# Performance work log

Measured on AMD Instinct MI355X. Metric: run time of the kernel, lower is better.

The kernel has to match this reference:

```python
import jax, jax.numpy as jnp
import numpy as np

B, T, C, H, W = 16, 128, 32, 16, 16
NUM_FEAT = 16
D = C * H * W            # conv1d in-channels (kernel size 1 => linear)
G = NUM_FEAT * H * W     # G3 out-channels


def setup_inputs() -> dict:
    key = jax.random.key(0)
    ks = jax.random.split(key, 8)
    s1 = 1.0 / np.sqrt(D)
    return {
        "input1": jax.random.normal(ks[0], (B, T, C, H, W), jnp.float32),
        "input2": jax.random.normal(ks[1], (B, T, C, H, W), jnp.float32),
        "w1": jax.random.uniform(ks[2], (NUM_FEAT, D), jnp.float32, -s1, s1),
        "b1": jax.random.uniform(ks[3], (NUM_FEAT,), jnp.float32, -s1, s1),
        "w2": jax.random.uniform(ks[4], (NUM_FEAT, D), jnp.float32, -s1, s1),
        "b2": jax.random.uniform(ks[5], (NUM_FEAT,), jnp.float32, -s1, s1),
        "w3": jax.random.uniform(ks[6], (G, D), jnp.float32, -s1, s1),
        "b3": jax.random.uniform(ks[7], (G,), jnp.float32, -s1, s1),
    }


def reference(input1, input2, w1, b1, w2, b2, w3, b3):
    b, t = input1.shape[:2]
    x1 = input1.reshape(b, t, D)  # [B,T,D]
    x2 = input2.reshape(b, t, D)
    # Conv1d(kernel=1) projections (channels-first conv == per-frame linear)
    q = jnp.einsum('btd,fd->btf', x1, w1) + b1          # [B,T,F]
    k = jnp.einsum('bsd,fd->bsf', x2, w2) + b2          # [B,S,F]
    scores = jnp.einsum('btf,bsf->bts', q, k)            # [B,T,T]
    attn = jax.nn.softmax(scores, axis=1)                # softmax over dim=1 (rows)
    v = jnp.einsum('bsd,gd->bsg', x1, w3) + b3           # [B,T,G]
    out = jnp.einsum('bts,bsg->btg', attn, v)            # [B,T,G]
    return out.reshape(b, t, NUM_FEAT, H, W)
```

## Files before the change

kernel.cpp:

```cpp
#include <hip/hip_runtime.h>
#include <cstdint>
#include <cstddef>

#define Bn 16
#define Tn 128
#define Dn 8192
#define Fn 16
#define Gn 4096
#define MT (Bn*Tn)

#define QKP 4

typedef __attribute__((ext_vector_type(8))) short short8;
typedef __attribute__((ext_vector_type(4))) float f32x4;

__device__ inline short f2bf(float f) {
    union { float f; uint32_t u; } c; c.f = f;
    uint32_t u = c.u;
    uint32_t r = (u + 0x7FFFu + ((u >> 16) & 1u)) >> 16;
    return (short)(r & 0xFFFFu);
}

__device__ inline short8 cvt8(float4 a, float4 b) {
    short8 v;
    v[0] = f2bf(a.x); v[1] = f2bf(a.y); v[2] = f2bf(a.z); v[3] = f2bf(a.w);
    v[4] = f2bf(b.x); v[5] = f2bf(b.y); v[6] = f2bf(b.z); v[7] = f2bf(b.w);
    return v;
}

#define N8_X1 (MT * Dn / 8)
#define N8_W3 ((size_t)Gn * Dn / 8)

__global__ __launch_bounds__(256) void cvt2_kernel(
    const float* __restrict__ x1, const float* __restrict__ w3,
    short* __restrict__ x1b, short* __restrict__ w3b)
{
    const size_t total = N8_X1 + N8_W3;
    size_t i = (size_t)blockIdx.x * 256 + threadIdx.x;
    const size_t stride = (size_t)gridDim.x * 256;
    for (; i < total; i += stride) {
        if (i < N8_X1) {
            const float4* s = ((const float4*)x1) + i * 2;
            ((short8*)x1b)[i] = cvt8(s[0], s[1]);
        } else {
            const size_t j = i - N8_X1;
            const float4* s = ((const float4*)w3) + j * 2;
            ((short8*)w3b)[j] = cvt8(s[0], s[1]);
        }
    }
}

__global__ __launch_bounds__(256) void qk_gemm_kernel(
    const short* __restrict__ x1b, const float* __restrict__ x2,
    const float* __restrict__ w1, const float* __restrict__ w2,
    float* __restrict__ qp, float* __restrict__ kp)
{
    __shared__ float red[4][16][16];
    const int tid = threadIdx.x;
    const int tile = blockIdx.x >> 1;
    const int isK  = blockIdx.x & 1;
    const int kq   = blockIdx.y;
    const int m0 = tile * 16;
    const int wave = tid >> 6, lane = tid & 63;
    const int quad = lane >> 4, r = lane & 15;
    const int kbase = kq * (Dn / QKP) + wave * (Dn / QKP / 4);

    f32x4 acc = {};

    if (!isK) {
        const short* ap = x1b + (size_t)(m0 + r) * Dn + kbase + quad * 8;
        const float* bp = w1 + (size_t)r * Dn + kbase + quad * 8;
        #pragma unroll 4
        for (int it = 0; it < 16; ++it) {
            short8 af = *(const short8*)(ap + it * 32);
            const float4* b4 = (const float4*)(bp + it * 32);
            short8 bf = cvt8(b4[0], b4[1]);
            acc = __builtin_amdgcn_mfma_f32_16x16x32_bf16(af, bf, acc, 0, 0, 0);
        }
    } else {
        const float* apf = x2 + (size_t)(m0 + r) * Dn + kbase + quad * 8;
        const float* bp  = w2 + (size_t)r * Dn + kbase + quad * 8;
        #pragma unroll 4
        for (int it = 0; it < 16; ++it) {
            const float4* a4 = (const float4*)(apf + it * 32);
            short8 af = cvt8(a4[0], a4[1]);
            const float4* b4 = (const float4*)(bp + it * 32);
            short8 bf = cvt8(b4[0], b4[1]);
            acc = __builtin_amdgcn_mfma_f32_16x16x32_bf16(af, bf, acc, 0, 0, 0);
        }
    }

    #pragma unroll
    for (int reg = 0; reg < 4; ++reg)
        red[wave][quad * 4 + reg][r] = acc[reg];
    __syncthreads();

    const int m = tid >> 4, f = tid & 15;
    float s = red[0][m][f] + red[1][m][f] + red[2][m][f] + red[3][m][f];
    float* dst = isK ? kp : qp;
    dst[((size_t)kq * MT + m0 + m) * Fn + f] = s;
}

__global__ __launch_bounds__(256) void attn_kernel(
    const float* __restrict__ qp, const float* __restrict__ kp,
    const float* __restrict__ b1, const float* __restrict__ b2,
    short* __restrict__ attn16)
{
    __shared__ float qs[Tn * 17];
    const int b = blockIdx.x;
    const int tid = threadIdx.x;
    const int wave = tid >> 6, lane = tid & 63;
    const int s = blockIdx.y * 4 + wave;

    for (int i = tid; i < Tn * Fn; i += 256) {
        float v = b1[i & 15];
        #pragma unroll
        for (int p = 0; p < QKP; ++p)
            v += qp[(size_t)p * MT * Fn + b * Tn * Fn + i];
        qs[(i >> 4) * 17 + (i & 15)] = v;
    }
    __syncthreads();

    float kr[16];
    #pragma unroll
    for (int f = 0; f < 16; ++f) {
        float v = b2[f];
        #pragma unroll
        for (int p = 0; p < QKP; ++p)
            v += kp[((size_t)p * MT + b * Tn + s) * Fn + f];
        kr[f] = v;
    }

    const int t0 = lane, t1 = lane + 64;
    float sc0 = 0.f, sc1 = 0.f;
    #pragma unroll
    for (int f = 0; f < 16; ++f) {
        sc0 += qs[t0 * 17 + f] * kr[f];
        sc1 += qs[t1 * 17 + f] * kr[f];
    }
    float m = fmaxf(sc0, sc1);
    #pragma unroll
    for (int off = 32; off > 0; off >>= 1)
        m = fmaxf(m, __shfl_xor(m, off, 64));
    const float e0 = __expf(sc0 - m), e1 = __expf(sc1 - m);
    float ssum = e0 + e1;
    #pragma unroll
    for (int off = 32; off > 0; off >>= 1)
        ssum += __shfl_xor(ssum, off, 64);
    const float inv = 1.f / ssum;

    short* ap = attn16 + (size_t)b * Tn * Tn;
    ap[t0 * Tn + s] = f2bf(e0 * inv);
    ap[t1 * Tn + s] = f2bf(e1 * inv);
}

#define BK 32

__global__ __launch_bounds__(256) void gemm_v_split_kernel(
    const short* __restrict__ A, const short* __restrict__ Bw,
    float* __restrict__ vTf, const int kspan)
{
    __shared__ __attribute__((aligned(16))) short As[128 * BK];
    __shared__ __attribute__((aligned(16))) short Bs[128 * BK];

    const int tid = threadIdx.x;
    const int m0 = blockIdx.y * 128;
    const int n0 = blockIdx.x * 128;
    const int z  = blockIdx.z;
    const int kbase = z * kspan;
    float* outp = vTf + (size_t)z * Gn * MT;
    const int wave = tid >> 6, lane = tid & 63;
    const int wm = (wave >> 1) * 64, wn = (wave & 1) * 64;
    const int quad = lane >> 4, r = lane & 15;

    const int srow = wave * 32 + (lane >> 2);
    const int scol = (lane & 3) * 8;
    const short* gA = A  + (size_t)(m0 + srow) * Dn + kbase + scol;
    const short* gB = Bw + (size_t)(n0 + srow) * Dn + kbase + scol;
    short* lA = &As[srow * BK + scol];
    short* lB = &Bs[srow * BK + scol];

    f32x4 acc[4][4] = {};

    #pragma unroll 1
    for (int k0 = 0; k0 < kspan; k0 += BK) {
        __syncthreads();
        __builtin_amdgcn_global_load_lds(
            (const __attribute__((address_space(1))) void*)(gA + k0),
            (__attribute__((address_space(3))) void*)lA, 16, 0, 0);
        __builtin_amdgcn_global_load_lds(
            (const __attribute__((address_space(1))) void*)(gA + k0 + (size_t)16 * Dn),
            (__attribute__((address_space(3))) void*)(lA + 16 * BK), 16, 0, 0);
        __builtin_amdgcn_global_load_lds(
            (const __attribute__((address_space(1))) void*)(gB + k0),
            (__attribute__((address_space(3))) void*)lB, 16, 0, 0);
        __builtin_amdgcn_global_load_lds(
            (const __attribute__((address_space(1))) void*)(gB + k0 + (size_t)16 * Dn),
            (__attribute__((address_space(3))) void*)(lB + 16 * BK), 16, 0, 0);
        __syncthreads();

        short8 af[4], bf[4];
        #pragma unroll
        for (int i = 0; i < 4; ++i)
            af[i] = *(const short8*)&As[(wm + i * 16 + r) * BK + quad * 8];
        #pragma unroll
        for (int j = 0; j < 4; ++j)
            bf[j] = *(const short8*)&Bs[(wn + j * 16 + r) * BK + quad * 8];

        #pragma unroll
        for (int i = 0; i < 4; ++i)
            #pragma unroll
            for (int j = 0; j < 4; ++j)
                acc[i][j] = __builtin_amdgcn_mfma_f32_16x16x32_bf16(
                    af[i], bf[j], acc[i][j], 0, 0, 0);
    }

    #pragma unroll
    for (int i = 0; i < 4; ++i) {
        #pragma unroll
        for (int reg = 0; reg < 4; ++reg) {
            const int rowg = m0 + wm + i * 16 + quad * 4 + reg;
            #pragma unroll
            for (int j = 0; j < 4; ++j) {
                const int col = n0 + wn + j * 16 + r;
                outp[(size_t)rowg * MT + col] = acc[i][j][reg];
            }
        }
    }
}

__global__ __launch_bounds__(256) void vt_cvt_kernel(
    const float* __restrict__ vTf, const float* __restrict__ bias,
    short* __restrict__ vT, const int nparts)
{
    const size_t N8 = (size_t)Gn * MT / 8;
    size_t i = (size_t)blockIdx.x * 256 + threadIdx.x;
    const size_t stride = (size_t)gridDim.x * 256;
    for (; i < N8; i += stride) {
        const float bv = bias[i >> 8];
        float4 a = {bv, bv, bv, bv}, b = {bv, bv, bv, bv};
        for (int p = 0; p < nparts; ++p) {
            const float4* pp = (const float4*)(vTf + (size_t)p * Gn * MT);
            float4 a1 = pp[i * 2], b1 = pp[i * 2 + 1];
            a.x += a1.x; a.y += a1.y; a.z += a1.z; a.w += a1.w;
            b.x += b1.x; b.y += b1.y; b.z += b1.z; b.w += b1.w;
        }
        ((short8*)vT)[i] = cvt8(a, b);
    }
}

__global__ __launch_bounds__(256) void gemm_v_kernel(
    const short* __restrict__ A, const short* __restrict__ Bw,
    const float* __restrict__ bias, short* __restrict__ vT)
{
    __shared__ __attribute__((aligned(16))) short As[128 * BK];
    __shared__ __attribute__((aligned(16))) short Bs[128 * BK];

    const int tid = threadIdx.x;
    const int m0 = blockIdx.y * 128;
    const int n0 = blockIdx.x * 128;
    const int wave = tid >> 6, lane = tid & 63;
    const int wm = (wave >> 1) * 64, wn = (wave & 1) * 64;
    const int quad = lane >> 4, r = lane & 15;

    const int srow = wave * 32 + (lane >> 2);
    const int scol = (lane & 3) * 8;
    const short* gA = A  + (size_t)(m0 + srow) * Dn + scol;
    const short* gB = Bw + (size_t)(n0 + srow) * Dn + scol;
    short* lA = &As[srow * BK + scol];
    short* lB = &Bs[srow * BK + scol];

    f32x4 acc[4][4] = {};

    #pragma unroll 1
    for (int k0 = 0; k0 < Dn; k0 += BK) {
        __syncthreads();
        __builtin_amdgcn_global_load_lds(
            (const __attribute__((address_space(1))) void*)(gA + k0),
            (__attribute__((address_space(3))) void*)lA, 16, 0, 0);
        __builtin_amdgcn_global_load_lds(
            (const __attribute__((address_space(1))) void*)(gA + k0 + (size_t)16 * Dn),
            (__attribute__((address_space(3))) void*)(lA + 16 * BK), 16, 0, 0);
        __builtin_amdgcn_global_load_lds(
            (const __attribute__((address_space(1))) void*)(gB + k0),
            (__attribute__((address_space(3))) void*)lB, 16, 0, 0);
        __builtin_amdgcn_global_load_lds(
            (const __attribute__((address_space(1))) void*)(gB + k0 + (size_t)16 * Dn),
            (__attribute__((address_space(3))) void*)(lB + 16 * BK), 16, 0, 0);
        __syncthreads();

        short8 af[4], bf[4];
        #pragma unroll
        for (int i = 0; i < 4; ++i)
            af[i] = *(const short8*)&As[(wm + i * 16 + r) * BK + quad * 8];
        #pragma unroll
        for (int j = 0; j < 4; ++j)
            bf[j] = *(const short8*)&Bs[(wn + j * 16 + r) * BK + quad * 8];

        #pragma unroll
        for (int i = 0; i < 4; ++i)
            #pragma unroll
            for (int j = 0; j < 4; ++j)
                acc[i][j] = __builtin_amdgcn_mfma_f32_16x16x32_bf16(
                    af[i], bf[j], acc[i][j], 0, 0, 0);
    }

    #pragma unroll
    for (int i = 0; i < 4; ++i) {
        #pragma unroll
        for (int reg = 0; reg < 4; ++reg) {
            const int rowg = m0 + wm + i * 16 + quad * 4 + reg;
            const float bv = bias[rowg];
            #pragma unroll
            for (int j = 0; j < 4; ++j) {
                const int col = n0 + wn + j * 16 + r;
                vT[(size_t)rowg * MT + col] = f2bf(acc[i][j][reg] + bv);
            }
        }
    }
}

__global__ __launch_bounds__(256) void out_gemm_kernel(
    const short* __restrict__ attn16, const short* __restrict__ vT,
    float* __restrict__ out)
{
    __shared__ __attribute__((aligned(16))) short As[128 * BK];
    __shared__ __attribute__((aligned(16))) short Bs[64 * BK];

    const int tid = threadIdx.x;
    const int b  = blockIdx.y;
    const int n0 = blockIdx.x * 64;
    const int wave = tid >> 6, lane = tid & 63;
    const int wm = (wave >> 1) * 64, wn = (wave & 1) * 32;
    const int quad = lane >> 4, r = lane & 15;

    const int srowA = wave * 32 + (lane >> 2);
    const int srowB = wave * 16 + (lane >> 2);
    const int scol = (lane & 3) * 8;
    const short* gA = attn16 + (size_t)b * Tn * Tn + srowA * Tn + scol;
    const short* gB = vT + (size_t)(n0 + srowB) * MT + b * Tn + scol;
    short* lA = &As[srowA * BK + scol];
    short* lB = &Bs[srowB * BK + scol];

    f32x4 acc[4][2] = {};

    #pragma unroll 1
    for (int k0 = 0; k0 < Tn; k0 += BK) {
        __syncthreads();
        __builtin_amdgcn_global_load_lds(
            (const __attribute__((address_space(1))) void*)(gA + k0),
            (__attribute__((address_space(3))) void*)lA, 16, 0, 0);
        __builtin_amdgcn_global_load_lds(
            (const __attribute__((address_space(1))) void*)(gA + k0 + 16 * Tn),
            (__attribute__((address_space(3))) void*)(lA + 16 * BK), 16, 0, 0);
        __builtin_amdgcn_global_load_lds(
            (const __attribute__((address_space(1))) void*)(gB + k0),
            (__attribute__((address_space(3))) void*)lB, 16, 0, 0);
        __syncthreads();

        short8 af[4], bf[2];
        #pragma unroll
        for (int i = 0; i < 4; ++i)
            af[i] = *(const short8*)&As[(wm + i * 16 + r) * BK + quad * 8];
        #pragma unroll
        for (int j = 0; j < 2; ++j)
            bf[j] = *(const short8*)&Bs[(wn + j * 16 + r) * BK + quad * 8];

        #pragma unroll
        for (int i = 0; i < 4; ++i)
            #pragma unroll
            for (int j = 0; j < 2; ++j)
                acc[i][j] = __builtin_amdgcn_mfma_f32_16x16x32_bf16(
                    af[i], bf[j], acc[i][j], 0, 0, 0);
    }

    #pragma unroll
    for (int j = 0; j < 2; ++j) {
        const int col = n0 + wn + j * 16 + r;
        #pragma unroll
        for (int i = 0; i < 4; ++i) {
            #pragma unroll
            for (int reg = 0; reg < 4; ++reg) {
                const int rowt = wm + i * 16 + quad * 4 + reg;
                out[((size_t)(b * Tn + rowt)) * Gn + col] = acc[i][j][reg];
            }
        }
    }
}

extern "C" void kernel_launch(void* const* d_in, const int* in_sizes, int n_in,
                              void* d_out, int out_size, void* d_ws, size_t ws_size,
                              hipStream_t stream)
{
    const float* x1 = (const float*)d_in[0];
    const float* x2 = (const float*)d_in[1];
    const float* w1 = (const float*)d_in[2];
    const float* b1 = (const float*)d_in[3];
    const float* w2 = (const float*)d_in[4];
    const float* b2 = (const float*)d_in[5];
    const float* w3 = (const float*)d_in[6];
    const float* b3 = (const float*)d_in[7];
    float* out = (float*)d_out;

    float* qp     = (float*)d_ws;
    float* kp     = qp + (size_t)QKP * MT * Fn;
    short* attn16 = (short*)(kp + (size_t)QKP * MT * Fn);
    short* vT     = attn16 + (size_t)Bn * Tn * Tn;
    short* x1b    = vT + (size_t)Gn * MT;
    short* w3b    = x1b + (size_t)MT * Dn;
    float* vTf    = (float*)(w3b + (size_t)Gn * Dn);

    const size_t base_need =
        (size_t)QKP * MT * Fn * 4 * 2 +
        (size_t)Bn * Tn * Tn * 2 +
        (size_t)Gn * MT * 2 +
        (size_t)MT * Dn * 2 +
        (size_t)Gn * Dn * 2;
    const size_t psize = (size_t)Gn * MT * 4;

    const int ksplit = (ws_size >= base_need + 2 * psize) ? 2 : 0;

    cvt2_kernel<<<4096, 256, 0, stream>>>(x1, w3, x1b, w3b);
    qk_gemm_kernel<<<dim3(256, QKP), 256, 0, stream>>>(x1b, x2, w1, w2, qp, kp);
    attn_kernel<<<dim3(Bn, Tn / 4), 256, 0, stream>>>(qp, kp, b1, b2, attn16);

    if (ksplit) {
        gemm_v_split_kernel<<<dim3(MT / 128, Gn / 128, ksplit), 256, 0, stream>>>(
            w3b, x1b, vTf, Dn / ksplit);
        vt_cvt_kernel<<<2048, 256, 0, stream>>>(vTf, b3, vT, ksplit);
    } else {
        gemm_v_kernel<<<dim3(MT / 128, Gn / 128), 256, 0, stream>>>(w3b, x1b, b3, vT);
    }

    out_gemm_kernel<<<dim3(Gn / 64, Bn), 256, 0, stream>>>(attn16, vT, out);
}
```

Baseline: 547.4 us.

## Double-buffer split-K V GEMM and fuse split reduction into output GEMM

The split-K V projection GEMM now double-buffers its LDS tiles, so the global-to-LDS loads for the next K step overlap the MFMA work on the current one. The separate vt_cvt reduction kernel is removed. The output GEMM instead reads both fp32 partials, adds the bias, and converts to bf16 while staging its B tile. This saves a kernel launch and a round trip of the bf16 vT buffer, but the fp32 partial reads move into the output GEMM's inner loop through plain register loads.

After: 522.0 us. -4.7%, faster.

```diff
diff --git a/kernel.cpp b/kernel.cpp
--- a/kernel.cpp
+++ b/kernel.cpp
@@ -160,8 +160,8 @@
     const short* __restrict__ A, const short* __restrict__ Bw,
     float* __restrict__ vTf, const int kspan)
 {
-    __shared__ __attribute__((aligned(16))) short As[128 * BK];
-    __shared__ __attribute__((aligned(16))) short Bs[128 * BK];
+    __shared__ __attribute__((aligned(16))) short As[2][128 * BK];
+    __shared__ __attribute__((aligned(16))) short Bs[2][128 * BK];
 
     const int tid = threadIdx.x;
     const int m0 = blockIdx.y * 128;
@@ -177,43 +177,57 @@
     const int scol = (lane & 3) * 8;
     const short* gA = A  + (size_t)(m0 + srow) * Dn + kbase + scol;
     const short* gB = Bw + (size_t)(n0 + srow) * Dn + kbase + scol;
-    short* lA = &As[srow * BK + scol];
-    short* lB = &Bs[srow * BK + scol];
 
     f32x4 acc[4][4] = {};
 
-    #pragma unroll 1
-    for (int k0 = 0; k0 < kspan; k0 += BK) {
-        __syncthreads();
-        __builtin_amdgcn_global_load_lds(
-            (const __attribute__((address_space(1))) void*)(gA + k0),
-            (__attribute__((address_space(3))) void*)lA, 16, 0, 0);
-        __builtin_amdgcn_global_load_lds(
-            (const __attribute__((address_space(1))) void*)(gA + k0 + (size_t)16 * Dn),
-            (__attribute__((address_space(3))) void*)(lA + 16 * BK), 16, 0, 0);
-        __builtin_amdgcn_global_load_lds(
-            (const __attribute__((address_space(1))) void*)(gB + k0),
-            (__attribute__((address_space(3))) void*)lB, 16, 0, 0);
-        __builtin_amdgcn_global_load_lds(
-            (const __attribute__((address_space(1))) void*)(gB + k0 + (size_t)16 * Dn),
-            (__attribute__((address_space(3))) void*)(lB + 16 * BK), 16, 0, 0);
-        __syncthreads();
-
-        short8 af[4], bf[4];
-        #pragma unroll
-        for (int i = 0; i < 4; ++i)
-            af[i] = *(const short8*)&As[(wm + i * 16 + r) * BK + quad * 8];
-        #pragma unroll
-        for (int j = 0; j < 4; ++j)
-            bf[j] = *(const short8*)&Bs[(wn + j * 16 + r) * BK + quad * 8];
-
-        #pragma unroll
-        for (int i = 0; i < 4; ++i)
-            #pragma unroll
-            for (int j = 0; j < 4; ++j)
-                acc[i][j] = __builtin_amdgcn_mfma_f32_16x16x32_bf16(
-                    af[i], bf[j], acc[i][j], 0, 0, 0);
-    }
+#define STAGE(buf, koff)                                                        \
+    do {                                                                        \
+        __builtin_amdgcn_global_load_lds(                                       \
+            (const __attribute__((address_space(1))) void*)(gA + (koff)),       \
+            (__attribute__((address_space(3))) void*)&As[buf][srow * BK + scol], 16, 0, 0); \
+        __builtin_amdgcn_global_load_lds(                                       \
+            (const __attribute__((address_space(1))) void*)(gA + (koff) + (size_t)16 * Dn), \
+            (__attribute__((address_space(3))) void*)&As[buf][(srow + 16) * BK + scol], 16, 0, 0); \
+        __builtin_amdgcn_global_load_lds(                                       \
+            (const __attribute__((address_space(1))) void*)(gB + (koff)),       \
+            (__attribute__((address_space(3))) void*)&Bs[buf][srow * BK + scol], 16, 0, 0); \
+        __builtin_amdgcn_global_load_lds(                                       \
+            (const __attribute__((address_space(1))) void*)(gB + (koff) + (size_t)16 * Dn), \
+            (__attribute__((address_space(3))) void*)&Bs[buf][(srow + 16) * BK + scol], 16, 0, 0); \
+    } while (0)
+
+#define COMPUTE(buf)                                                            \
+    do {                                                                        \
+        short8 af[4], bf[4];                                                    \
+        _Pragma("unroll")                                                       \
+        for (int i = 0; i < 4; ++i)                                             \
+            af[i] = *(const short8*)&As[buf][(wm + i * 16 + r) * BK + quad * 8];\
+        _Pragma("unroll")                                                       \
+        for (int j = 0; j < 4; ++j)                                             \
+            bf[j] = *(const short8*)&Bs[buf][(wn + j * 16 + r) * BK + quad * 8];\
+        _Pragma("unroll")                                                       \
+        for (int i = 0; i < 4; ++i)                                             \
+            _Pragma("unroll")                                                   \
+            for (int j = 0; j < 4; ++j)                                         \
+                acc[i][j] = __builtin_amdgcn_mfma_f32_16x16x32_bf16(            \
+                    af[i], bf[j], acc[i][j], 0, 0, 0);                          \
+    } while (0)
+
+    STAGE(0, 0);
+    __syncthreads();
+
+    int cur = 0;
+    #pragma unroll 2
+    for (int k0 = BK; k0 < kspan; k0 += BK) {
+        STAGE(cur ^ 1, k0);
+        COMPUTE(cur);
+        __syncthreads();
+        cur ^= 1;
+    }
+    COMPUTE(cur);
+
+#undef STAGE
+#undef COMPUTE
 
     #pragma unroll
     for (int i = 0; i < 4; ++i) {
@@ -226,26 +240,6 @@
                 outp[(size_t)rowg * MT + col] = acc[i][j][reg];
             }
         }
-    }
-}
-
-__global__ __launch_bounds__(256) void vt_cvt_kernel(
-    const float* __restrict__ vTf, const float* __restrict__ bias,
-    short* __restrict__ vT, const int nparts)
-{
-    const size_t N8 = (size_t)Gn * MT / 8;
-    size_t i = (size_t)blockIdx.x * 256 + threadIdx.x;
-    const size_t stride = (size_t)gridDim.x * 256;
-    for (; i < N8; i += stride) {
-        const float bv = bias[i >> 8];
-        float4 a = {bv, bv, bv, bv}, b = {bv, bv, bv, bv};
-        for (int p = 0; p < nparts; ++p) {
-            const float4* pp = (const float4*)(vTf + (size_t)p * Gn * MT);
-            float4 a1 = pp[i * 2], b1 = pp[i * 2 + 1];
-            a.x += a1.x; a.y += a1.y; a.z += a1.z; a.w += a1.w;
-            b.x += b1.x; b.y += b1.y; b.z += b1.z; b.w += b1.w;
-        }
-        ((short8*)vT)[i] = cvt8(a, b);
     }
 }
 
@@ -315,6 +309,80 @@
             for (int j = 0; j < 4; ++j) {
                 const int col = n0 + wn + j * 16 + r;
                 vT[(size_t)rowg * MT + col] = f2bf(acc[i][j][reg] + bv);
+            }
+        }
+    }
+}
+
+__global__ __launch_bounds__(256) void out_gemm_fused_kernel(
+    const short* __restrict__ attn16, const float* __restrict__ vTf,
+    const float* __restrict__ b3, float* __restrict__ out)
+{
+    __shared__ __attribute__((aligned(16))) short As[128 * BK];
+    __shared__ __attribute__((aligned(16))) short Bs[64 * BK];
+
+    const int tid = threadIdx.x;
+    const int b  = blockIdx.y;
+    const int n0 = blockIdx.x * 64;
+    const int wave = tid >> 6, lane = tid & 63;
+    const int wm = (wave >> 1) * 64, wn = (wave & 1) * 32;
+    const int quad = lane >> 4, r = lane & 15;
+
+    const int srowA = wave * 32 + (lane >> 2);
+    const int srowB = wave * 16 + (lane >> 2);
+    const int scol = (lane & 3) * 8;
+    const short* gA = attn16 + (size_t)b * Tn * Tn + srowA * Tn + scol;
+    const float* gB0 = vTf + (size_t)(n0 + srowB) * MT + b * Tn + scol;
+    const float* gB1 = gB0 + (size_t)Gn * MT;
+    const float bv = b3[n0 + srowB];
+    short* lA = &As[srowA * BK + scol];
+
+    f32x4 acc[4][2] = {};
+
+    #pragma unroll 1
+    for (int k0 = 0; k0 < Tn; k0 += BK) {
+        __syncthreads();
+        __builtin_amdgcn_global_load_lds(
+            (const __attribute__((address_space(1))) void*)(gA + k0),
+            (__attribute__((address_space(3))) void*)lA, 16, 0, 0);
+        __builtin_amdgcn_global_load_lds(
+            (const __attribute__((address_space(1))) void*)(gA + k0 + 16 * Tn),
+            (__attribute__((address_space(3))) void*)(lA + 16 * BK), 16, 0, 0);
+        {
+            const float4* p0 = (const float4*)(gB0 + k0);
+            const float4* p1 = (const float4*)(gB1 + k0);
+            float4 a0 = p0[0], a1 = p0[1], c0 = p1[0], c1 = p1[1];
+            a0.x += c0.x + bv; a0.y += c0.y + bv; a0.z += c0.z + bv; a0.w += c0.w + bv;
+            a1.x += c1.x + bv; a1.y += c1.y + bv; a1.z += c1.z + bv; a1.w += c1.w + bv;
+            *(short8*)&Bs[srowB * BK + scol] = cvt8(a0, a1);
+        }
+        __syncthreads();
+
+        short8 af[4], bf[2];
+        #pragma unroll
+        for (int i = 0; i < 4; ++i)
+            af[i] = *(const short8*)&As[(wm + i * 16 + r) * BK + quad * 8];
+        #pragma unroll
+        for (int j = 0; j < 2; ++j)
+            bf[j] = *(const short8*)&Bs[(wn + j * 16 + r) * BK + quad * 8];
+
+        #pragma unroll
+        for (int i = 0; i < 4; ++i)
+            #pragma unroll
+            for (int j = 0; j < 2; ++j)
+                acc[i][j] = __builtin_amdgcn_mfma_f32_16x16x32_bf16(
+                    af[i], bf[j], acc[i][j], 0, 0, 0);
+    }
+
+    #pragma unroll
+    for (int j = 0; j < 2; ++j) {
+        const int col = n0 + wn + j * 16 + r;
+        #pragma unroll
+        for (int i = 0; i < 4; ++i) {
+            #pragma unroll
+            for (int reg = 0; reg < 4; ++reg) {
+                const int rowt = wm + i * 16 + quad * 4 + reg;
+                out[((size_t)(b * Tn + rowt)) * Gn + col] = acc[i][j][reg];
             }
         }
     }
@@ -425,12 +493,12 @@
     attn_kernel<<<dim3(Bn, Tn / 4), 256, 0, stream>>>(qp, kp, b1, b2, attn16);
 
     if (ksplit) {
-        gemm_v_split_kernel<<<dim3(MT / 128, Gn / 128, ksplit), 256, 0, stream>>>(
-            w3b, x1b, vTf, Dn / ksplit);
-        vt_cvt_kernel<<<2048, 256, 0, stream>>>(vTf, b3, vT, ksplit);
+        gemm_v_split_kernel<<<dim3(MT / 128, Gn / 128, 2), 256, 0, stream>>>(
+            w3b, x1b, vTf, Dn / 2);
+        out_gemm_fused_kernel<<<dim3(Gn / 64, Bn), 256, 0, stream>>>(
+            attn16, vTf, b3, out);
     } else {
         gemm_v_kernel<<<dim3(MT / 128, Gn / 128), 256, 0, stream>>>(w3b, x1b, b3, vT);
-    }
-
-    out_gemm_kernel<<<dim3(Gn / 64, Bn), 256, 0, stream>>>(attn16, vT, out);
-}
+        out_gemm_kernel<<<dim3(Gn / 64, Bn), 256, 0, stream>>>(attn16, vT, out);
+    }
+}
```
